# Performance work log

Measured on AMD Instinct MI355X. Metric: run time of the kernel, lower is better.

Reference implementation:

```python
import jax, jax.numpy as jnp
import numpy as np

N = 50000   # nodes
E = 640000  # edges
IN = 256    # in_dim
H = 128     # hidden
OUT = 40    # out_dim
EPS = 1e-5  # BatchNorm eps


def setup_inputs() -> dict:
    key = jax.random.key(0)
    ks = jax.random.split(key, 14)
    x = jax.random.normal(ks[0], (N, IN), jnp.float32)
    edge_index = jax.random.randint(ks[1], (2, E), 0, N)
    def lin(k, fan_in, shape):
        return jax.random.normal(k, shape, jnp.float32) / np.float32(np.sqrt(fan_in))
    return {
        "x": x,
        "edge_index": edge_index,
        # block 0 (256 -> 128, has res_proj)
        "W0": lin(ks[2], IN, (IN, H)),
        "b0": jnp.zeros((H,), jnp.float32),
        "g0": jnp.ones((H,), jnp.float32),
        "be0": jnp.zeros((H,), jnp.float32),
        "pW": lin(ks[3], IN, (IN, H)),
        "pb": jnp.zeros((H,), jnp.float32),
        # block 1 (128 -> 128, identity residual)
        "W1": lin(ks[4], H, (H, H)),
        "b1": jnp.zeros((H,), jnp.float32),
        "g1": jnp.ones((H,), jnp.float32),
        "be1": jnp.zeros((H,), jnp.float32),
        # head
        "hW": lin(ks[5], H, (H, OUT)),
        "hb": jnp.zeros((OUT,), jnp.float32),
    }


def _gcn_conv(x, W, b, edge_index):
    """GCNConv(improved=True): x' = D^-1/2 (A + 2I) D^-1/2 (x W) + b."""
    h = x @ W  # [N, dout]
    row, col = edge_index[0], edge_index[1]  # source -> target
    # degree of A + 2I (edge_weight = 1, self-loop fill = 2.0)
    deg = jnp.zeros((N,), h.dtype).at[col].add(1.0) + 2.0
    dis = jax.lax.rsqrt(deg)  # deg > 0 always (self-loops)
    norm = dis[row] * dis[col]  # [E]
    # neighbor aggregation: scatter-add normalized messages to targets
    agg = jnp.zeros_like(h).at[col].add(norm[:, None] * h[row])
    # self-loop contribution with weight 2.0
    agg = agg + (2.0 * dis * dis)[:, None] * h
    return agg + b


def _bn(x, gamma, beta):
    # batch statistics (training-mode BatchNorm math), biased variance
    m = jnp.mean(x, axis=0)
    v = jnp.mean(jnp.square(x - m), axis=0)
    return (x - m) * jax.lax.rsqrt(v + EPS) * gamma + beta


def reference(x, edge_index, W0, b0, g0, be0, pW, pb, W1, b1, g1, be1, hW, hb):
    # block 0: conv -> bn -> relu -> (+ res_proj(x))
    out = jax.nn.relu(_bn(_gcn_conv(x, W0, b0, edge_index), g0, be0))
    x1 = out + (x @ pW + pb)
    # block 1: conv -> bn -> relu -> (+ identity)
    out = jax.nn.relu(_bn(_gcn_conv(x1, W1, b1, edge_index), g1, be1))
    x2 = out + x1
    return x2 @ hW + hb  # [N, OUT]
```

## Files before the change

kernel.cpp:

```cpp
#include <hip/hip_runtime.h>

#define H 128
#define IN_DIM 256
#define OUT_DIM 40
#define EPS 1e-5f

typedef unsigned short ushortT;
typedef __attribute__((ext_vector_type(8))) short bf16x8;
typedef __attribute__((ext_vector_type(4))) float f32x4;

static __device__ __forceinline__ ushortT f2bf(float f) {
    union { float f; unsigned u; } v; v.f = f;
    unsigned r = v.u + 0x7FFF + ((v.u >> 16) & 1);
    return (ushortT)(r >> 16);
}
static __device__ __forceinline__ unsigned pk2(float a, float b) {
    return (unsigned)f2bf(a) | ((unsigned)f2bf(b) << 16);
}
static __device__ __forceinline__ float bflo(unsigned v) {
    union { unsigned u; float f; } t; t.u = v << 16; return t.f;
}
static __device__ __forceinline__ float bfhi(unsigned v) {
    union { unsigned u; float f; } t; t.u = v & 0xFFFF0000u; return t.f;
}


__global__ __launch_bounds__(256) void count_kernel(const int* __restrict__ ei, int E, int* __restrict__ cnt) {
    int e = blockIdx.x * 256 + threadIdx.x;
    if (e < E) atomicAdd(&cnt[ei[E + e]], 1);
}

__global__ __launch_bounds__(256) void scan_block_sum(const int* __restrict__ cnt, int* __restrict__ bsum,
                                                      float* __restrict__ dis, int N) {
    __shared__ int s[256];
    int i = blockIdx.x * 256 + threadIdx.x;
    int v = (i < N) ? cnt[i] : 0;
    if (i < N) dis[i] = rsqrtf((float)v + 2.0f);
    s[threadIdx.x] = v;
    __syncthreads();
    for (int o = 128; o > 0; o >>= 1) {
        if (threadIdx.x < o) s[threadIdx.x] += s[threadIdx.x + o];
        __syncthreads();
    }
    if (threadIdx.x == 0) bsum[blockIdx.x] = s[0];
}

__global__ void scan_tops(const int* __restrict__ bsum, int* __restrict__ boff, int* __restrict__ rowptrN, int nb) {
    __shared__ int s[256];
    int t = threadIdx.x;
    int v = (t < nb) ? bsum[t] : 0;
    s[t] = v;
    __syncthreads();
    for (int o = 1; o < 256; o <<= 1) {
        int u = (t >= o) ? s[t - o] : 0;
        __syncthreads();
        s[t] += u;
        __syncthreads();
    }
    if (t < nb) boff[t] = s[t] - v;
    if (t == 255) *rowptrN = s[255];
}

__global__ __launch_bounds__(256) void scan_final(const int* __restrict__ cnt, const int* __restrict__ boff,
                                                  int* __restrict__ rowptr, int* __restrict__ cursor, int N) {
    __shared__ int s[256];
    int t = threadIdx.x;
    int i = blockIdx.x * 256 + t;
    int v = (i < N) ? cnt[i] : 0;
    s[t] = v;
    __syncthreads();
    for (int o = 1; o < 256; o <<= 1) {
        int u = (t >= o) ? s[t - o] : 0;
        __syncthreads();
        s[t] += u;
        __syncthreads();
    }
    if (i < N) {
        int e = boff[blockIdx.x] + s[t] - v;
        rowptr[i] = e;
        cursor[i] = e;
    }
}

__global__ __launch_bounds__(256) void fill_kernel(const int* __restrict__ ei, int E,
                                                   int* __restrict__ cursor, int* __restrict__ eidx) {
    int e = blockIdx.x * 256 + threadIdx.x;
    if (e < E) {
        int r = ei[e], c = ei[E + e];
        int slot = atomicAdd(&cursor[c], 1);
        eidx[slot] = r;
    }
}


__global__ __launch_bounds__(256) void prep_weights(const float* __restrict__ W0, const float* __restrict__ pW,
                                                    const float* __restrict__ W1, const float* __restrict__ hW,
                                                    ushortT* __restrict__ Wt0, ushortT* __restrict__ WtP,
                                                    ushortT* __restrict__ Wt1, ushortT* __restrict__ WtH) {
    int i = blockIdx.x * 256 + threadIdx.x;
    if (i < 32768) { int n = i >> 8, k = i & 255; Wt0[i] = f2bf(W0[k * 128 + n]); WtP[i] = f2bf(pW[k * 128 + n]); }
    if (i < 16384) { int n = i >> 7, k = i & 127; Wt1[i] = f2bf(W1[k * 128 + n]); }
    if (i < 6144)  { int n = i >> 7, k = i & 127; WtH[i] = (n < OUT_DIM) ? f2bf(hW[k * OUT_DIM + n]) : (ushortT)0; }
}


template <int K, bool DUAL, bool ABF16>
__global__ __launch_bounds__(256) void mgemm(const float* __restrict__ Xf,
                                             const ushortT* __restrict__ Xb,
                                             const ushortT* __restrict__ WtA,
                                             const ushortT* __restrict__ WtB,
                                             const float* __restrict__ biasB,
                                             ushortT* __restrict__ OA,
                                             ushortT* __restrict__ OB,
                                             int N) {
    __shared__ __align__(16) ushortT As[64][40];
    __shared__ __align__(16) ushortT Bs[DUAL ? 2 : 1][128][40];

    int tid = threadIdx.x;
    int brow = blockIdx.x * 64;
    int w = tid >> 6, lane = tid & 63;
    int lm = lane & 15, lk = lane >> 4;

    f32x4 accA[4][2];
    f32x4 accB[4][2];
#pragma unroll
    for (int mt = 0; mt < 4; ++mt)
#pragma unroll
        for (int nt = 0; nt < 2; ++nt) { accA[mt][nt] = (f32x4)0.f; accB[mt][nt] = (f32x4)0.f; }

    for (int kc = 0; kc < K; kc += 32) {
        __syncthreads();
        if constexpr (!ABF16) {
            int row = tid >> 2, q = tid & 3;
            int gr = brow + row;
            float4 v0 = make_float4(0.f, 0.f, 0.f, 0.f), v1 = v0;
            if (gr < N) {
                const float4* p = (const float4*)&Xf[(size_t)gr * K + kc + q * 8];
                v0 = p[0]; v1 = p[1];
            }
            uint4 pkv;
            pkv.x = pk2(v0.x, v0.y);
            pkv.y = pk2(v0.z, v0.w);
            pkv.z = pk2(v1.x, v1.y);
            pkv.w = pk2(v1.z, v1.w);
            *(uint4*)&As[row][q * 8] = pkv;
        } else {
            int row = tid >> 2, q = tid & 3;
            int gr = brow + row;
            uint4 v = make_uint4(0u, 0u, 0u, 0u);
            if (gr < N) v = *(const uint4*)&Xb[(size_t)gr * K + kc + q * 8];
            *(uint4*)&As[row][q * 8] = v;
        }
        if constexpr (DUAL) {
            int mat = tid >> 7, n = tid & 127;
            const ushortT* Wt = mat ? WtB : WtA;
            const uint4* src = (const uint4*)&Wt[(size_t)n * K + kc];
            uint4 a = src[0], b = src[1], c = src[2], d = src[3];
            uint4* dst = (uint4*)&Bs[mat][n][0];
            dst[0] = a; dst[1] = b; dst[2] = c; dst[3] = d;
        } else {
            int n = tid >> 1, hf = tid & 1;
            const uint4* src = (const uint4*)&WtA[(size_t)n * K + kc + hf * 16];
            uint4 a = src[0], b = src[1];
            uint4* dst = (uint4*)&Bs[0][n][hf * 16];
            dst[0] = a; dst[1] = b;
        }
        __syncthreads();

        bf16x8 af[4];
#pragma unroll
        for (int mt = 0; mt < 4; ++mt)
            af[mt] = *(const bf16x8*)&As[mt * 16 + lm][lk * 8];
#pragma unroll
        for (int nt = 0; nt < 2; ++nt) {
            bf16x8 b0 = *(const bf16x8*)&Bs[0][w * 32 + nt * 16 + lm][lk * 8];
#pragma unroll
            for (int mt = 0; mt < 4; ++mt)
                accA[mt][nt] = __builtin_amdgcn_mfma_f32_16x16x32_bf16(af[mt], b0, accA[mt][nt], 0, 0, 0);
            if constexpr (DUAL) {
                bf16x8 b1 = *(const bf16x8*)&Bs[1][w * 32 + nt * 16 + lm][lk * 8];
#pragma unroll
                for (int mt = 0; mt < 4; ++mt)
                    accB[mt][nt] = __builtin_amdgcn_mfma_f32_16x16x32_bf16(af[mt], b1, accB[mt][nt], 0, 0, 0);
            }
        }
    }

    float bb[2] = {0.f, 0.f};
    if constexpr (DUAL) {
#pragma unroll
        for (int nt = 0; nt < 2; ++nt) bb[nt] = biasB[w * 32 + nt * 16 + lm];
    }
#pragma unroll
    for (int mt = 0; mt < 4; ++mt) {
        int r0 = brow + mt * 16 + lk * 4;
#pragma unroll
        for (int nt = 0; nt < 2; ++nt) {
            int col = w * 32 + nt * 16 + lm;
#pragma unroll
            for (int j = 0; j < 4; ++j) {
                int r = r0 + j;
                if (r < N) {
                    OA[(size_t)r * 128 + col] = f2bf(accA[mt][nt][j]);
                    if constexpr (DUAL) OB[(size_t)r * 128 + col] = f2bf(accB[mt][nt][j] + bb[nt]);
                }
            }
        }
    }
}


__global__ __launch_bounds__(256) void aggregate_bf(const ushortT* __restrict__ h,
                                                    const int* __restrict__ rowptr,
                                                    const int* __restrict__ eidx,
                                                    const float* __restrict__ dis,
                                                    ushortT* __restrict__ aggb, int N) {
    int n = blockIdx.x * 4 + (threadIdx.x >> 6);
    int lane = threadIdx.x & 63;
    if (n >= N) return;
    int beg = rowptr[n], end = rowptr[n + 1];
    float dn = dis[n];
    const unsigned* h1 = (const unsigned*)h;
    float a0x = 0.f, a0y = 0.f, a1x = 0.f, a1y = 0.f;
    float a2x = 0.f, a2y = 0.f, a3x = 0.f, a3y = 0.f;
    int p = beg;
    for (; p + 3 < end; p += 4) {
        int s0 = eidx[p], s1 = eidx[p + 1], s2 = eidx[p + 2], s3 = eidx[p + 3];
        float n0 = dis[s0] * dn, n1 = dis[s1] * dn, n2 = dis[s2] * dn, n3 = dis[s3] * dn;
        unsigned v0 = h1[(size_t)s0 * 64 + lane];
        unsigned v1 = h1[(size_t)s1 * 64 + lane];
        unsigned v2 = h1[(size_t)s2 * 64 + lane];
        unsigned v3 = h1[(size_t)s3 * 64 + lane];
        a0x = fmaf(n0, bflo(v0), a0x); a0y = fmaf(n0, bfhi(v0), a0y);
        a1x = fmaf(n1, bflo(v1), a1x); a1y = fmaf(n1, bfhi(v1), a1y);
        a2x = fmaf(n2, bflo(v2), a2x); a2y = fmaf(n2, bfhi(v2), a2y);
        a3x = fmaf(n3, bflo(v3), a3x); a3y = fmaf(n3, bfhi(v3), a3y);
    }
    for (; p < end; ++p) {
        int s0 = eidx[p];
        float n0 = dis[s0] * dn;
        unsigned v0 = h1[(size_t)s0 * 64 + lane];
        a0x = fmaf(n0, bflo(v0), a0x); a0y = fmaf(n0, bfhi(v0), a0y);
    }
    {
        unsigned v = h1[(size_t)n * 64 + lane];
        float sw = 2.f * dn * dn;
        a0x = fmaf(sw, bflo(v), a0x); a0y = fmaf(sw, bfhi(v), a0y);
    }
    float rx = (a0x + a1x) + (a2x + a3x);
    float ry = (a0y + a1y) + (a2y + a3y);
    ((unsigned*)aggb)[(size_t)n * 64 + lane] = pk2(rx, ry);
}


__global__ __launch_bounds__(256) void stats_bf(const unsigned* __restrict__ v, int totalU,
                                                float* __restrict__ sums) {
    int tid = blockIdx.x * 256 + threadIdx.x;
    int stride = gridDim.x * 256;
    float sx = 0.f, sy = 0.f, qx = 0.f, qy = 0.f;
    for (int i = tid; i < totalU; i += stride) {
        unsigned u = v[i];
        float a = bflo(u), b = bfhi(u);
        sx += a; sy += b;
        qx = fmaf(a, a, qx); qy = fmaf(b, b, qy);
    }
    __shared__ float l0[256], l1[256], l2[256], l3[256];
    int t = threadIdx.x;
    l0[t] = sx; l1[t] = sy; l2[t] = qx; l3[t] = qy;
    __syncthreads();
    if (t < 64) {
        sx = (l0[t] + l0[t + 64]) + (l0[t + 128] + l0[t + 192]);
        sy = (l1[t] + l1[t + 64]) + (l1[t + 128] + l1[t + 192]);
        qx = (l2[t] + l2[t + 64]) + (l2[t + 128] + l2[t + 192]);
        qy = (l3[t] + l3[t + 64]) + (l3[t + 128] + l3[t + 192]);
        atomicAdd(&sums[2 * t], sx);
        atomicAdd(&sums[2 * t + 1], sy);
        atomicAdd(&sums[128 + 2 * t], qx);
        atomicAdd(&sums[128 + 2 * t + 1], qy);
    }
}


__global__ __launch_bounds__(256) void bn_relu_add_v3(const uint2* __restrict__ aggb,
                                                      const float* __restrict__ stats,
                                                      const float* __restrict__ g,
                                                      const float* __restrict__ be,
                                                      const uint2* __restrict__ projb,
                                                      uint2* __restrict__ x1b, int N) {
    __shared__ float sc[128], sh[128];
    int t = threadIdx.x;
    if (t < 128) {
        float mean = stats[t] / (float)N;
        float var = stats[128 + t] / (float)N - mean * mean;
        float inv = rsqrtf(var + EPS);
        float s = g[t] * inv;
        sc[t] = s;
        sh[t] = be[t] - mean * s;
    }
    __syncthreads();
    size_t i2 = (size_t)blockIdx.x * 256 + t;
    size_t total2 = (size_t)N * 32;
    if (i2 >= total2) return;
    int ch = (int)(i2 & 31) * 4;
    uint2 a = aggb[i2];
    uint2 d = projb[i2];
    float v0 = fmaxf(fmaf(bflo(a.x), sc[ch + 0], sh[ch + 0]), 0.f) + bflo(d.x);
    float v1 = fmaxf(fmaf(bfhi(a.x), sc[ch + 1], sh[ch + 1]), 0.f) + bfhi(d.x);
    float v2 = fmaxf(fmaf(bflo(a.y), sc[ch + 2], sh[ch + 2]), 0.f) + bflo(d.y);
    float v3 = fmaxf(fmaf(bfhi(a.y), sc[ch + 3], sh[ch + 3]), 0.f) + bfhi(d.y);
    uint2 r;
    r.x = pk2(v0, v1);
    r.y = pk2(v2, v3);
    x1b[i2] = r;
}


__global__ __launch_bounds__(256) void head_fused(const uint4* __restrict__ aggb,
                                                  const uint4* __restrict__ x1b,
                                                  const float* __restrict__ stats,
                                                  const float* __restrict__ g,
                                                  const float* __restrict__ be,
                                                  const ushortT* __restrict__ WtH,
                                                  const float* __restrict__ hb,
                                                  float* __restrict__ out, int N) {
    __shared__ __align__(16) ushortT As[64][136];
    __shared__ __align__(16) ushortT Bs[48][136];
    __shared__ float sc[128], sh[128];

    int tid = threadIdx.x;
    int brow = blockIdx.x * 64;
    int w = tid >> 6, lane = tid & 63;
    int lm = lane & 15, lk = lane >> 4;

    if (tid < 128) {
        float mean = stats[tid] / (float)N;
        float var = stats[128 + tid] / (float)N - mean * mean;
        float inv = rsqrtf(var + EPS);
        float s = g[tid] * inv;
        sc[tid] = s;
        sh[tid] = be[tid] - mean * s;
    }
    if (tid < 192) {
        int row = tid >> 2, q = tid & 3;
        const uint4* src = (const uint4*)&WtH[(size_t)row * H + q * 32];
        uint4 a = src[0], b = src[1], c = src[2], d = src[3];
        uint4* dst = (uint4*)&Bs[row][q * 32];
        dst[0] = a; dst[1] = b; dst[2] = c; dst[3] = d;
    }
    __syncthreads();
#pragma unroll
    for (int k = 0; k < 4; ++k) {
        int idx = k * 256 + tid;
        int row = idx >> 4, colq = idx & 15;
        int gr = brow + row;
        uint4 a = make_uint4(0u, 0u, 0u, 0u), x = a;
        if (gr < N) {
            size_t gidx = (size_t)brow * 16 + idx;
            a = aggb[gidx];
            x = x1b[gidx];
        }
        int ch = colq * 8;
        float v0 = fmaxf(fmaf(bflo(a.x), sc[ch + 0], sh[ch + 0]), 0.f) + bflo(x.x);
        float v1 = fmaxf(fmaf(bfhi(a.x), sc[ch + 1], sh[ch + 1]), 0.f) + bfhi(x.x);
        float v2 = fmaxf(fmaf(bflo(a.y), sc[ch + 2], sh[ch + 2]), 0.f) + bflo(x.y);
        float v3 = fmaxf(fmaf(bfhi(a.y), sc[ch + 3], sh[ch + 3]), 0.f) + bfhi(x.y);
        float v4 = fmaxf(fmaf(bflo(a.z), sc[ch + 4], sh[ch + 4]), 0.f) + bflo(x.z);
        float v5 = fmaxf(fmaf(bfhi(a.z), sc[ch + 5], sh[ch + 5]), 0.f) + bfhi(x.z);
        float v6 = fmaxf(fmaf(bflo(a.w), sc[ch + 6], sh[ch + 6]), 0.f) + bflo(x.w);
        float v7 = fmaxf(fmaf(bfhi(a.w), sc[ch + 7], sh[ch + 7]), 0.f) + bfhi(x.w);
        uint4 pv;
        pv.x = pk2(v0, v1);
        pv.y = pk2(v2, v3);
        pv.z = pk2(v4, v5);
        pv.w = pk2(v6, v7);
        *(uint4*)&As[row][colq * 8] = pv;
    }
    __syncthreads();

    f32x4 acc[3];
#pragma unroll
    for (int nt = 0; nt < 3; ++nt) acc[nt] = (f32x4)0.f;
#pragma unroll
    for (int ks = 0; ks < 4; ++ks) {
        bf16x8 a = *(const bf16x8*)&As[w * 16 + lm][ks * 32 + lk * 8];
#pragma unroll
        for (int nt = 0; nt < 3; ++nt) {
            bf16x8 b = *(const bf16x8*)&Bs[nt * 16 + lm][ks * 32 + lk * 8];
            acc[nt] = __builtin_amdgcn_mfma_f32_16x16x32_bf16(a, b, acc[nt], 0, 0, 0);
        }
    }
#pragma unroll
    for (int nt = 0; nt < 3; ++nt) {
        int col = nt * 16 + lm;
        if (col < OUT_DIM) {
            float bbv = hb[col];
#pragma unroll
            for (int j = 0; j < 4; ++j) {
                int r = brow + w * 16 + lk * 4 + j;
                if (r < N) out[(size_t)r * OUT_DIM + col] = acc[nt][j] + bbv;
            }
        }
    }
}


extern "C" void kernel_launch(void* const* d_in, const int* in_sizes, int n_in,
                              void* d_out, int out_size, void* d_ws, size_t ws_size,
                              hipStream_t stream) {
    const float* x   = (const float*)d_in[0];
    const int*   ei  = (const int*)d_in[1];
    const float* W0  = (const float*)d_in[2];
    const float* g0  = (const float*)d_in[4];
    const float* be0 = (const float*)d_in[5];
    const float* pW  = (const float*)d_in[6];
    const float* pb  = (const float*)d_in[7];
    const float* W1  = (const float*)d_in[8];
    const float* g1  = (const float*)d_in[10];
    const float* be1 = (const float*)d_in[11];
    const float* hW  = (const float*)d_in[12];
    const float* hb  = (const float*)d_in[13];
    float* out = (float*)d_out;

    int N = in_sizes[0] / IN_DIM;
    int E = in_sizes[1] / 2;
    size_t NH = (size_t)N * H;

    ushortT* hb16   = (ushortT*)d_ws;
    ushortT* aggb   = hb16 + NH;
    ushortT* projb  = aggb + NH;
    ushortT* x1b    = projb + NH;
    float*   dis    = (float*)(x1b + NH);
    int*     cnt    = (int*)(dis + N);
    int*     rowptr = cnt + N;
    int*     cursor = rowptr + (N + 1);
    int*     eidx   = cursor + N;
    float*   stats  = (float*)(eidx + E);
    ushortT* Wt0    = (ushortT*)(stats + 256);
    ushortT* WtP    = Wt0 + 128 * 256;
    ushortT* Wt1    = WtP + 128 * 256;
    ushortT* WtH    = Wt1 + 128 * 128;
    int*     bsum   = (int*)(WtH + 48 * 128);
    int*     boff   = bsum + 256;

    int gE = (E + 255) / 256;
    int nb = (N + 255) / 256;
    int gRows = (N + 63) / 64;
    int gAgg = (N + 3) / 4;
    int gNH2 = (int)((NH / 4 + 255) / 256);

    hipMemsetAsync(cnt, 0, (size_t)N * sizeof(int), stream);
    prep_weights<<<128, 256, 0, stream>>>(W0, pW, W1, hW, Wt0, WtP, Wt1, WtH);
    count_kernel<<<gE, 256, 0, stream>>>(ei, E, cnt);
    scan_block_sum<<<nb, 256, 0, stream>>>(cnt, bsum, dis, N);
    scan_tops<<<1, 256, 0, stream>>>(bsum, boff, &rowptr[N], nb);
    scan_final<<<nb, 256, 0, stream>>>(cnt, boff, rowptr, cursor, N);
    fill_kernel<<<gE, 256, 0, stream>>>(ei, E, cursor, eidx);

    mgemm<IN_DIM, true, false><<<gRows, 256, 0, stream>>>(x, nullptr, Wt0, WtP, pb, hb16, projb, N);
    aggregate_bf<<<gAgg, 256, 0, stream>>>(hb16, rowptr, eidx, dis, aggb, N);
    hipMemsetAsync(stats, 0, 256 * sizeof(float), stream);
    stats_bf<<<256, 256, 0, stream>>>((const unsigned*)aggb, (int)(NH / 2), stats);
    bn_relu_add_v3<<<gNH2, 256, 0, stream>>>((const uint2*)aggb, stats, g0, be0,
                                             (const uint2*)projb, (uint2*)x1b, N);

    mgemm<H, false, true><<<gRows, 256, 0, stream>>>(nullptr, x1b, Wt1, nullptr, nullptr, hb16, nullptr, N);
    aggregate_bf<<<gAgg, 256, 0, stream>>>(hb16, rowptr, eidx, dis, aggb, N);
    hipMemsetAsync(stats, 0, 256 * sizeof(float), stream);
    stats_bf<<<256, 256, 0, stream>>>((const unsigned*)aggb, (int)(NH / 2), stats);

    head_fused<<<gRows, 256, 0, stream>>>((const uint4*)aggb, (const uint4*)x1b, stats, g1, be1,
                                          WtH, hb, out, N);
}
```

Measured before the change: 279.5 us.

## Partition CSR fill by XCD and restructure GEMMs with register-resident weights

The CSR fill kernel now has each block scan a chunk of edges and handle only the target nodes that belong to its XCD slice (blockIdx & 7). The intent is to keep atomic cursor updates local to one XCD's L2, at the cost of every edge being read eight times. Both GEMMs are rewritten as 512-thread kernels that stage the whole A row tile in shared memory once and read weight fragments directly from global memory into registers. This removes the per-K-chunk shared-memory staging and barriers. In the first GEMM, separate waves now compute the conv weight and the projection weight instead of one wave doing both.

Result: no change. 274.2 us (-1.9%).

```diff
diff --git a/kernel.cpp b/kernel.cpp
--- a/kernel.cpp
+++ b/kernel.cpp
@@ -82,13 +82,20 @@
     }
 }
 
-__global__ __launch_bounds__(256) void fill_kernel(const int* __restrict__ ei, int E,
-                                                   int* __restrict__ cursor, int* __restrict__ eidx) {
-    int e = blockIdx.x * 256 + threadIdx.x;
-    if (e < E) {
-        int r = ei[e], c = ei[E + e];
-        int slot = atomicAdd(&cursor[c], 1);
-        eidx[slot] = r;
+__global__ __launch_bounds__(256) void fill_xcd(const int* __restrict__ ei, int E, int nper,
+                                                int* __restrict__ cursor, int* __restrict__ eidx) {
+    int xcd = blockIdx.x & 7;
+    int nchunk = gridDim.x >> 3;
+    int chunk = blockIdx.x >> 3;
+    int csz = (E + nchunk - 1) / nchunk;
+    int beg = chunk * csz;
+    int end = min(E, beg + csz);
+    for (int e = beg + (int)threadIdx.x; e < end; e += 256) {
+        int c = ei[E + e];
+        if (c / nper == xcd) {
+            int slot = atomicAdd(&cursor[c], 1);
+            eidx[slot] = ei[e];
+        }
     }
 }
 
@@ -104,109 +111,146 @@
 }
 
 
-template <int K, bool DUAL, bool ABF16>
-__global__ __launch_bounds__(256) void mgemm(const float* __restrict__ Xf,
-                                             const ushortT* __restrict__ Xb,
-                                             const ushortT* __restrict__ WtA,
-                                             const ushortT* __restrict__ WtB,
-                                             const float* __restrict__ biasB,
-                                             ushortT* __restrict__ OA,
-                                             ushortT* __restrict__ OB,
-                                             int N) {
-    __shared__ __align__(16) ushortT As[64][40];
-    __shared__ __align__(16) ushortT Bs[DUAL ? 2 : 1][128][40];
-
+__global__ __launch_bounds__(512) void mgemm0(const float* __restrict__ X,
+                                              const ushortT* __restrict__ Wt0,
+                                              const ushortT* __restrict__ WtP,
+                                              const float* __restrict__ pb,
+                                              ushortT* __restrict__ Oh,
+                                              ushortT* __restrict__ Op,
+                                              int N) {
+    __shared__ __align__(16) ushortT As[64][264];
     int tid = threadIdx.x;
     int brow = blockIdx.x * 64;
+
+#pragma unroll
+    for (int i = 0; i < 8; ++i) {
+        int idx = i * 512 + tid;
+        int row = idx >> 6, c4 = idx & 63;
+        int gr = brow + row;
+        float4 v = make_float4(0.f, 0.f, 0.f, 0.f);
+        if (gr < N) v = *(const float4*)&X[(size_t)gr * IN_DIM + c4 * 4];
+        uint2 p;
+        p.x = pk2(v.x, v.y);
+        p.y = pk2(v.z, v.w);
+        *(uint2*)&As[row][c4 * 4] = p;
+    }
+    __syncthreads();
+
     int w = tid >> 6, lane = tid & 63;
     int lm = lane & 15, lk = lane >> 4;
-
-    f32x4 accA[4][2];
-    f32x4 accB[4][2];
+    int mat = w >> 2;
+    int colbase = (w & 3) * 32;
+    const ushortT* Wt = mat ? WtP : Wt0;
+
+    f32x4 acc[4][2];
 #pragma unroll
     for (int mt = 0; mt < 4; ++mt)
 #pragma unroll
-        for (int nt = 0; nt < 2; ++nt) { accA[mt][nt] = (f32x4)0.f; accB[mt][nt] = (f32x4)0.f; }
-
-    for (int kc = 0; kc < K; kc += 32) {
-        __syncthreads();
-        if constexpr (!ABF16) {
-            int row = tid >> 2, q = tid & 3;
-            int gr = brow + row;
-            float4 v0 = make_float4(0.f, 0.f, 0.f, 0.f), v1 = v0;
-            if (gr < N) {
-                const float4* p = (const float4*)&Xf[(size_t)gr * K + kc + q * 8];
-                v0 = p[0]; v1 = p[1];
+        for (int nt = 0; nt < 2; ++nt) acc[mt][nt] = (f32x4)0.f;
+
+#pragma unroll
+    for (int kc = 0; kc < 2; ++kc) {
+        bf16x8 breg[2][4];
+#pragma unroll
+        for (int nt = 0; nt < 2; ++nt)
+#pragma unroll
+            for (int ks = 0; ks < 4; ++ks)
+                breg[nt][ks] = *(const bf16x8*)&Wt[(size_t)(colbase + nt * 16 + lm) * IN_DIM + kc * 128 + ks * 32 + lk * 8];
+#pragma unroll
+        for (int ks = 0; ks < 4; ++ks) {
+            bf16x8 af[4];
+#pragma unroll
+            for (int mt = 0; mt < 4; ++mt)
+                af[mt] = *(const bf16x8*)&As[mt * 16 + lm][kc * 128 + ks * 32 + lk * 8];
+#pragma unroll
+            for (int nt = 0; nt < 2; ++nt)
+#pragma unroll
+                for (int mt = 0; mt < 4; ++mt)
+                    acc[mt][nt] = __builtin_amdgcn_mfma_f32_16x16x32_bf16(af[mt], breg[nt][ks], acc[mt][nt], 0, 0, 0);
+        }
+    }
+
+    float bb[2] = {0.f, 0.f};
+    if (mat) {
+        bb[0] = pb[colbase + lm];
+        bb[1] = pb[colbase + 16 + lm];
+    }
+    ushortT* O = mat ? Op : Oh;
+#pragma unroll
+    for (int mt = 0; mt < 4; ++mt)
+#pragma unroll
+        for (int nt = 0; nt < 2; ++nt) {
+            int col = colbase + nt * 16 + lm;
+#pragma unroll
+            for (int j = 0; j < 4; ++j) {
+                int r = brow + mt * 16 + lk * 4 + j;
+                if (r < N) O[(size_t)r * 128 + col] = f2bf(acc[mt][nt][j] + bb[nt]);
             }
-            uint4 pkv;
-            pkv.x = pk2(v0.x, v0.y);
-            pkv.y = pk2(v0.z, v0.w);
-            pkv.z = pk2(v1.x, v1.y);
-            pkv.w = pk2(v1.z, v1.w);
-            *(uint4*)&As[row][q * 8] = pkv;
-        } else {
-            int row = tid >> 2, q = tid & 3;
-            int gr = brow + row;
-            uint4 v = make_uint4(0u, 0u, 0u, 0u);
-            if (gr < N) v = *(const uint4*)&Xb[(size_t)gr * K + kc + q * 8];
-            *(uint4*)&As[row][q * 8] = v;
-        }
-        if constexpr (DUAL) {
-            int mat = tid >> 7, n = tid & 127;
-            const ushortT* Wt = mat ? WtB : WtA;
-            const uint4* src = (const uint4*)&Wt[(size_t)n * K + kc];
-            uint4 a = src[0], b = src[1], c = src[2], d = src[3];
-            uint4* dst = (uint4*)&Bs[mat][n][0];
-            dst[0] = a; dst[1] = b; dst[2] = c; dst[3] = d;
-        } else {
-            int n = tid >> 1, hf = tid & 1;
-            const uint4* src = (const uint4*)&WtA[(size_t)n * K + kc + hf * 16];
-            uint4 a = src[0], b = src[1];
-            uint4* dst = (uint4*)&Bs[0][n][hf * 16];
-            dst[0] = a; dst[1] = b;
-        }
-        __syncthreads();
-
+        }
+}
+
+
+__global__ __launch_bounds__(512) void mgemm1(const ushortT* __restrict__ Xb,
+                                              const ushortT* __restrict__ Wt1,
+                                              ushortT* __restrict__ O,
+                                              int N) {
+    __shared__ __align__(16) ushortT As[128][136];
+    int tid = threadIdx.x;
+    int brow = blockIdx.x * 128;
+
+#pragma unroll
+    for (int i = 0; i < 4; ++i) {
+        int idx = i * 512 + tid;
+        int row = idx >> 4, q = idx & 15;
+        int gr = brow + row;
+        uint4 v = make_uint4(0u, 0u, 0u, 0u);
+        if (gr < N) v = *(const uint4*)&Xb[(size_t)gr * H + q * 8];
+        *(uint4*)&As[row][q * 8] = v;
+    }
+    __syncthreads();
+
+    int w = tid >> 6, lane = tid & 63;
+    int lm = lane & 15, lk = lane >> 4;
+    int rh = (w >> 2) * 64;
+    int colbase = (w & 3) * 32;
+
+    bf16x8 breg[2][4];
+#pragma unroll
+    for (int nt = 0; nt < 2; ++nt)
+#pragma unroll
+        for (int ks = 0; ks < 4; ++ks)
+            breg[nt][ks] = *(const bf16x8*)&Wt1[(size_t)(colbase + nt * 16 + lm) * H + ks * 32 + lk * 8];
+
+    f32x4 acc[4][2];
+#pragma unroll
+    for (int mt = 0; mt < 4; ++mt)
+#pragma unroll
+        for (int nt = 0; nt < 2; ++nt) acc[mt][nt] = (f32x4)0.f;
+
+#pragma unroll
+    for (int ks = 0; ks < 4; ++ks) {
         bf16x8 af[4];
 #pragma unroll
         for (int mt = 0; mt < 4; ++mt)
-            af[mt] = *(const bf16x8*)&As[mt * 16 + lm][lk * 8];
+            af[mt] = *(const bf16x8*)&As[rh + mt * 16 + lm][ks * 32 + lk * 8];
+#pragma unroll
+        for (int nt = 0; nt < 2; ++nt)
+#pragma unroll
+            for (int mt = 0; mt < 4; ++mt)
+                acc[mt][nt] = __builtin_amdgcn_mfma_f32_16x16x32_bf16(af[mt], breg[nt][ks], acc[mt][nt], 0, 0, 0);
+    }
+
+#pragma unroll
+    for (int mt = 0; mt < 4; ++mt)
 #pragma unroll
         for (int nt = 0; nt < 2; ++nt) {
-            bf16x8 b0 = *(const bf16x8*)&Bs[0][w * 32 + nt * 16 + lm][lk * 8];
-#pragma unroll
-            for (int mt = 0; mt < 4; ++mt)
-                accA[mt][nt] = __builtin_amdgcn_mfma_f32_16x16x32_bf16(af[mt], b0, accA[mt][nt], 0, 0, 0);
-            if constexpr (DUAL) {
-                bf16x8 b1 = *(const bf16x8*)&Bs[1][w * 32 + nt * 16 + lm][lk * 8];
-#pragma unroll
-                for (int mt = 0; mt < 4; ++mt)
-                    accB[mt][nt] = __builtin_amdgcn_mfma_f32_16x16x32_bf16(af[mt], b1, accB[mt][nt], 0, 0, 0);
+            int col = colbase + nt * 16 + lm;
+#pragma unroll
+            for (int j = 0; j < 4; ++j) {
+                int r = brow + rh + mt * 16 + lk * 4 + j;
+                if (r < N) O[(size_t)r * 128 + col] = f2bf(acc[mt][nt][j]);
             }
         }
-    }
-
-    float bb[2] = {0.f, 0.f};
-    if constexpr (DUAL) {
-#pragma unroll
-        for (int nt = 0; nt < 2; ++nt) bb[nt] = biasB[w * 32 + nt * 16 + lm];
-    }
-#pragma unroll
-    for (int mt = 0; mt < 4; ++mt) {
-        int r0 = brow + mt * 16 + lk * 4;
-#pragma unroll
-        for (int nt = 0; nt < 2; ++nt) {
-            int col = w * 32 + nt * 16 + lm;
-#pragma unroll
-            for (int j = 0; j < 4; ++j) {
-                int r = r0 + j;
-                if (r < N) {
-                    OA[(size_t)r * 128 + col] = f2bf(accA[mt][nt][j]);
-                    if constexpr (DUAL) OB[(size_t)r * 128 + col] = f2bf(accB[mt][nt][j] + bb[nt]);
-                }
-            }
-        }
-    }
 }
 
 
@@ -444,7 +488,8 @@
 
     int gE = (E + 255) / 256;
     int nb = (N + 255) / 256;
-    int gRows = (N + 63) / 64;
+    int g64 = (N + 63) / 64;
+    int g128 = (N + 127) / 128;
     int gAgg = (N + 3) / 4;
     int gNH2 = (int)((NH / 4 + 255) / 256);
 
@@ -454,20 +499,20 @@
     scan_block_sum<<<nb, 256, 0, stream>>>(cnt, bsum, dis, N);
     scan_tops<<<1, 256, 0, stream>>>(bsum, boff, &rowptr[N], nb);
     scan_final<<<nb, 256, 0, stream>>>(cnt, boff, rowptr, cursor, N);
-    fill_kernel<<<gE, 256, 0, stream>>>(ei, E, cursor, eidx);
-
-    mgemm<IN_DIM, true, false><<<gRows, 256, 0, stream>>>(x, nullptr, Wt0, WtP, pb, hb16, projb, N);
+    fill_xcd<<<2048, 256, 0, stream>>>(ei, E, (N + 7) / 8, cursor, eidx);
+
+    mgemm0<<<g64, 512, 0, stream>>>(x, Wt0, WtP, pb, hb16, projb, N);
     aggregate_bf<<<gAgg, 256, 0, stream>>>(hb16, rowptr, eidx, dis, aggb, N);
     hipMemsetAsync(stats, 0, 256 * sizeof(float), stream);
     stats_bf<<<256, 256, 0, stream>>>((const unsigned*)aggb, (int)(NH / 2), stats);
     bn_relu_add_v3<<<gNH2, 256, 0, stream>>>((const uint2*)aggb, stats, g0, be0,
                                              (const uint2*)projb, (uint2*)x1b, N);
 
-    mgemm<H, false, true><<<gRows, 256, 0, stream>>>(nullptr, x1b, Wt1, nullptr, nullptr, hb16, nullptr, N);
+    mgemm1<<<g128, 512, 0, stream>>>(x1b, Wt1, hb16, N);
     aggregate_bf<<<gAgg, 256, 0, stream>>>(hb16, rowptr, eidx, dis, aggb, N);
     hipMemsetAsync(stats, 0, 256 * sizeof(float), stream);
     stats_bf<<<256, 256, 0, stream>>>((const unsigned*)aggb, (int)(NH / 2), stats);
 
-    head_fused<<<gRows, 256, 0, stream>>>((const uint4*)aggb, (const uint4*)x1b, stats, g1, be1,
-                                          WtH, hb, out, N);
-}
+    head_fused<<<g64, 256, 0, stream>>>((const uint4*)aggb, (const uint4*)x1b, stats, g1, be1,
+                                        WtH, hb, out, N);
+}
```
